# Optimization experiments

Measured on AMD Instinct MI355X. Metric: run time of the kernel, lower is better.

## Reference

```python
import jax, jax.numpy as jnp
import numpy as np

EPS = 1e-5

def setup_inputs() -> dict:
    key = jax.random.key(0)
    k1, k2, k3 = jax.random.split(key, 3)
    B, D, H = 8192, 1536, 16384
    x = jax.random.normal(k1, (B, D), dtype=jnp.float32)
    # torch Linear default init ~ U(-1/sqrt(fan_in), 1/sqrt(fan_in)); scaled normal is fine for a reference
    W_enc = jax.random.normal(k2, (H, D), dtype=jnp.float32) * (1.0 / np.sqrt(D))
    W_dec = jax.random.normal(k3, (D, H), dtype=jnp.float32) * (1.0 / np.sqrt(H))
    pre_bias = jnp.zeros((D,), dtype=jnp.float32)
    latent_bias = jnp.zeros((H,), dtype=jnp.float32)
    return {"x": x, "W_enc": W_enc, "W_dec": W_dec,
            "pre_bias": pre_bias, "latent_bias": latent_bias, "k": 64}


def reference(x, W_enc, W_dec, pre_bias, latent_bias, k):
    # ---- LN preprocess (torch .std uses Bessel correction, ddof=1) ----
    mu = jnp.mean(x, axis=-1, keepdims=True)          # [B,1]
    xc = x - mu
    std = jnp.std(xc, axis=-1, keepdims=True, ddof=1)  # [B,1]
    xn = xc / (std + EPS)

    # ---- encode: Linear(bias=False) on (xn - pre_bias), add latent_bias ----
    h = jnp.einsum('bd,hd->bh', xn - pre_bias, W_enc) + latent_bias  # [B,H]
    h = jax.nn.relu(h)

    # ---- topk sparsity: keep values >= k-th largest per row ----
    topk_vals = jax.lax.top_k(h, k)[0]                # [B,k]
    threshold = topk_vals[:, -1:]                     # [B,1]
    h_sparse = h * (h >= threshold)

    # ---- decode + denormalize ----
    recon = jnp.einsum('bh,dh->bd', h_sparse, W_dec) + pre_bias
    recon = recon * std + mu

    # ---- metrics (as arrays instead of .item()) ----
    sparsity_ratio = jnp.mean(jnp.mean((h_sparse == 0).astype(jnp.float32), axis=1))
    abs_h = jnp.abs(h_sparse)
    mean_activation = jnp.mean(abs_h)
    std_activation = jnp.std(abs_h, ddof=1)
    return recon, h_sparse, sparsity_ratio, mean_activation, std_activation
```

## Files before the change

kernel.cpp:

```cpp
#include <hip/hip_runtime.h>
#include <hip/hip_bf16.h>
#include <math.h>

static constexpr int Bn = 8192;
static constexpr int Hn = 16384;
static constexpr int Dn = 1536;
static constexpr int KTOP = 64;
static constexpr int KE = 1536;
static constexpr int WSTR = 2048;
static constexpr double EPSD = 1e-5;

static constexpr size_t MU_OFF  = 0;
static constexpr size_t STD_OFF = 32768;
static constexpr size_t CNT_OFF = 98304;
static constexpr size_t NNZ_OFF = 131072;
static constexpr size_t SUM_OFF = 131200;
static constexpr size_t MUD_OFF = 262144;
static constexpr size_t RID_OFF = 327680;
static constexpr size_t IDX_OFF = (size_t)1 << 20;
static constexpr size_t VAL_OFF = (size_t)6 << 20;
static constexpr size_t AP_OFF  = (size_t)16 << 20;
static constexpr size_t BP_OFF  = (size_t)48 << 20;
static constexpr size_t WT_OFF  = (size_t)104 << 20;
static constexpr size_t H16_OFF = (size_t)176 << 20;

typedef __attribute__((ext_vector_type(8))) short short8;
typedef __attribute__((ext_vector_type(4))) float f32x4;

static __device__ __forceinline__ unsigned short f2bf(float f) {
    __hip_bfloat16 b = __float2bfloat16(f);
    return *reinterpret_cast<unsigned short*>(&b);
}
static __device__ __forceinline__ float bf2f(unsigned short u) {
    return __uint_as_float(((unsigned)u) << 16);
}
static __device__ __forceinline__ void gload_lds16(const void* g, void* l) {
    __builtin_amdgcn_global_load_lds(
        (const __attribute__((address_space(1))) unsigned int*)g,
        (__attribute__((address_space(3))) unsigned int*)l, 16, 0, 0);
}

__global__ void k_zero(unsigned* nnz, double* sums) {
    if (threadIdx.x == 0) { *nnz = 0u; sums[0] = 0.0; sums[1] = 0.0; }
}

__global__ __launch_bounds__(256) void k_rowstats(const float* __restrict__ x,
                                                  const float* __restrict__ pre_bias,
                                                  double* __restrict__ muD,
                                                  double* __restrict__ rinvD,
                                                  float* __restrict__ muF,
                                                  float* __restrict__ stdF,
                                                  unsigned short* __restrict__ Ap) {
    const int row = blockIdx.x;
    const int tid = threadIdx.x;
    const float* xr = x + (size_t)row * Dn;
    float v[6];
#pragma unroll
    for (int i = 0; i < 6; ++i) v[i] = xr[tid + 256 * i];
    double s = 0.0;
#pragma unroll
    for (int i = 0; i < 6; ++i) s += (double)v[i];
    __shared__ double redD[4];
    __shared__ double smu, srin;
#pragma unroll
    for (int o = 32; o > 0; o >>= 1) s += __shfl_down(s, o);
    if ((tid & 63) == 0) redD[tid >> 6] = s;
    __syncthreads();
    if (tid == 0) smu = (redD[0] + redD[1] + redD[2] + redD[3]) / (double)Dn;
    __syncthreads();
    const double m = smu;
    double q = 0.0;
#pragma unroll
    for (int i = 0; i < 6; ++i) { double d = (double)v[i] - m; q += d * d; }
#pragma unroll
    for (int o = 32; o > 0; o >>= 1) q += __shfl_down(q, o);
    if ((tid & 63) == 0) redD[tid >> 6] = q;
    __syncthreads();
    if (tid == 0) {
        double var = (redD[0] + redD[1] + redD[2] + redD[3]) / (double)(Dn - 1);
        double sd = sqrt(var);
        muD[row] = m;
        srin = 1.0 / (sd + EPSD);
        rinvD[row] = srin;
        muF[row] = (float)m;
        stdF[row] = (float)sd;
    }
    __syncthreads();
    const double ri = srin;
    unsigned short* ar = Ap + (size_t)row * KE;
#pragma unroll
    for (int i = 0; i < 6; ++i) {
        const int d = tid + i * 256;
        double a = ((double)v[i] - m) * ri - (double)pre_bias[d];
        ar[d] = f2bf((float)a);
    }
}

__global__ __launch_bounds__(256) void k_splitW(const float* __restrict__ Wenc,
                                                unsigned short* __restrict__ Bp) {
    const int row = blockIdx.x;
    const int tid = threadIdx.x;
    const float2* wr = (const float2*)(Wenc + (size_t)row * Dn);
    ushort2* br = (ushort2*)(Bp + (size_t)row * KE);
#pragma unroll
    for (int i = 0; i < 3; ++i) {
        float2 w = wr[tid + i * 256];
        ushort2 o; o.x = f2bf(w.x); o.y = f2bf(w.y);
        br[tid + i * 256] = o;
    }
}

__global__ __launch_bounds__(256) void k_transpose(const float* __restrict__ Wdec,
                                                   unsigned short* __restrict__ WdecT) {
    __shared__ float tile[32][33];
    const int h0 = blockIdx.x * 32;
    const int d0 = blockIdx.y * 32;
    const int tx = threadIdx.x & 31;
    const int ty = threadIdx.x >> 5;
#pragma unroll
    for (int r = 0; r < 4; ++r) {
        int d = ty + r * 8;
        tile[d][tx] = Wdec[(size_t)(d0 + d) * Hn + h0 + tx];
    }
    __syncthreads();
#pragma unroll
    for (int r = 0; r < 4; ++r) {
        int h = ty + r * 8;
        WdecT[(size_t)(h0 + h) * WSTR + d0 + tx] = f2bf(tile[tx][h]);
    }
}

__global__ __launch_bounds__(256) void k_gemm(const unsigned short* __restrict__ Ap,
                                              const unsigned short* __restrict__ Bp,
                                              const float* __restrict__ lat_bias,
                                              unsigned short* __restrict__ hout16) {
    __shared__ unsigned short As[128 * 64];
    __shared__ unsigned short Bs[128 * 64];
    const int tid = threadIdx.x;
    const int lane = tid & 63;
    const int w = tid >> 6;
    const int wm = w >> 1, wn = w & 1;

    const int nwg = (Bn / 128) * (Hn / 128);
    int swz = (blockIdx.x % 8) * (nwg / 8) + blockIdx.x / 8;
    int st = swz >> 6;
    int wi = swz & 63;
    int stm = st >> 4, stn = st & 15;
    const int bm = stm * 8 + (wi >> 3);
    const int bn = stn * 8 + (wi & 7);

    const int sr = tid >> 3;
    const int sp = tid & 7;
    const int ssl = sp ^ (sr & 7);
    const size_t arow0 = (size_t)(bm * 128) * KE;
    const size_t brow0 = (size_t)(bn * 128) * KE;

    f32x4 acc[4][4];
#pragma unroll
    for (int i = 0; i < 4; ++i)
#pragma unroll
        for (int j = 0; j < 4; ++j) acc[i][j] = (f32x4){0.f, 0.f, 0.f, 0.f};

    constexpr int NT = KE / 64;
    for (int t = 0; t < NT; ++t) {
        const int k0 = t * 64;
#pragma unroll
        for (int i = 0; i < 4; ++i) {
            gload_lds16(Ap + arow0 + (size_t)(i * 32 + sr) * KE + k0 + ssl * 8,
                        (char*)As + i * 4096 + tid * 16);
            gload_lds16(Bp + brow0 + (size_t)(i * 32 + sr) * KE + k0 + ssl * 8,
                        (char*)Bs + i * 4096 + tid * 16);
        }
        __syncthreads();
#pragma unroll
        for (int kk = 0; kk < 2; ++kk) {
            short8 af[4], bf[4];
#pragma unroll
            for (int f = 0; f < 4; ++f) {
                const int ar = wm * 64 + f * 16 + (lane & 15);
                const int aslot = (kk * 4 + (lane >> 4)) ^ (ar & 7);
                af[f] = *(const short8*)((const char*)As + ar * 128 + aslot * 16);
                const int brr = wn * 64 + f * 16 + (lane & 15);
                const int bslot = (kk * 4 + (lane >> 4)) ^ (brr & 7);
                bf[f] = *(const short8*)((const char*)Bs + brr * 128 + bslot * 16);
            }
#pragma unroll
            for (int fi = 0; fi < 4; ++fi)
#pragma unroll
                for (int fj = 0; fj < 4; ++fj)
                    acc[fi][fj] = __builtin_amdgcn_mfma_f32_16x16x32_bf16(
                        af[fi], bf[fj], acc[fi][fj], 0, 0, 0);
        }
        __syncthreads();
    }

    const int col = lane & 15;
    float biasv[4];
#pragma unroll
    for (int fj = 0; fj < 4; ++fj)
        biasv[fj] = lat_bias[bn * 128 + wn * 64 + fj * 16 + col];
#pragma unroll
    for (int fi = 0; fi < 4; ++fi) {
        const int gm0 = bm * 128 + wm * 64 + fi * 16 + (lane >> 4) * 4;
#pragma unroll
        for (int fj = 0; fj < 4; ++fj) {
            const int gn = bn * 128 + wn * 64 + fj * 16 + col;
#pragma unroll
            for (int r = 0; r < 4; ++r) {
                float vv = acc[fi][fj][r] + biasv[fj];
                hout16[(size_t)(gm0 + r) * Hn + gn] = f2bf(fmaxf(vv, 0.f));
            }
        }
    }
}

__global__ __launch_bounds__(256) void k_topsel(const unsigned short* __restrict__ h16,
                                                const float* __restrict__ x,
                                                const float* __restrict__ Wenc,
                                                const float* __restrict__ pre_bias,
                                                const float* __restrict__ lat_bias,
                                                const double* __restrict__ muD,
                                                const double* __restrict__ rinvD,
                                                unsigned* __restrict__ counts,
                                                int* __restrict__ idx_list,
                                                float* __restrict__ val_list) {
    const int row = blockIdx.x;
    const int tid = threadIdx.x;
    const int lane = tid & 63;
    const int wid = tid >> 6;
    const unsigned short* hr16 = h16 + (size_t)row * Hn;
    const unsigned* hu = (const unsigned*)hr16;
    unsigned u[32];
#pragma unroll
    for (int j = 0; j < 32; ++j) u[j] = hu[j * 256 + tid];

    __shared__ int wsum[4];
    __shared__ unsigned sbc;
    unsigned lo = 0, hi = 0xFFFFu;
    while (lo < hi) {
        const unsigned mid = (lo + hi + 1) >> 1;
        int c = 0;
#pragma unroll
        for (int j = 0; j < 32; ++j) {
            c += ((u[j] & 0xFFFFu) >= mid) ? 1 : 0;
            c += ((u[j] >> 16) >= mid) ? 1 : 0;
        }
#pragma unroll
        for (int o = 32; o > 0; o >>= 1) c += __shfl_down(c, o);
        if ((tid & 63) == 0) wsum[tid >> 6] = c;
        __syncthreads();
        if (tid == 0) sbc = (unsigned)(wsum[0] + wsum[1] + wsum[2] + wsum[3]);
        __syncthreads();
        if (sbc >= (unsigned)KTOP) lo = mid; else hi = mid - 1;
    }
    const float thr = bf2f((unsigned short)lo);
    const float DELTA = 0.02f;
    const float hi_t = thr + DELTA;
    const float lo_t = thr - DELTA;

    constexpr int MAXC = 128;
    __shared__ int s_g, s_c;
    __shared__ int cidx[MAXC];
    __shared__ double cvalD[MAXC];
    __shared__ float cref[MAXC];
    __shared__ unsigned char csel[MAXC];
    __shared__ unsigned long long kmask[256];
    __shared__ unsigned ccnt[256];
    __shared__ unsigned cinc[256];
    if (tid == 0) { s_g = 0; s_c = 0; }
    __syncthreads();
    int g_loc = 0;
#pragma unroll
    for (int j = 0; j < 32; ++j) {
        float v0 = bf2f((unsigned short)(u[j] & 0xFFFFu));
        float v1 = bf2f((unsigned short)(u[j] >> 16));
        const int i0 = 2 * (j * 256 + tid);
        if (v0 > hi_t) g_loc++;
        else if (v0 >= lo_t) {
            int p = atomicAdd(&s_c, 1);
            if (p < MAXC) cidx[p] = i0;
        }
        if (v1 > hi_t) g_loc++;
        else if (v1 >= lo_t) {
            int p = atomicAdd(&s_c, 1);
            if (p < MAXC) cidx[p] = i0 + 1;
        }
    }
    if (g_loc) atomicAdd(&s_g, g_loc);
    __syncthreads();
    const int ec = (s_c < MAXC) ? s_c : MAXC;

    {
        const double rmu = muD[row];
        const double rin = rinvD[row];
        const float* xr = x + (size_t)row * Dn;
        for (int e = wid; e < ec; e += 4) {
            const int feat = cidx[e];
            const float* wr = Wenc + (size_t)feat * Dn;
            double acc = 0.0;
            for (int d = lane; d < Dn; d += 64) {
                double xn = ((double)xr[d] - rmu) * rin - (double)pre_bias[d];
                acc = fma(xn, (double)wr[d], acc);
            }
#pragma unroll
            for (int o = 32; o > 0; o >>= 1) acc += __shfl_down(acc, o);
            if (lane == 0) {
                double hv = acc + (double)lat_bias[feat];
                cvalD[e] = hv;
                float hf = (float)hv;
                cref[e] = hf > 0.f ? hf : 0.f;
            }
        }
    }
    __syncthreads();
    if (tid == 0) {
        const int need = KTOP - s_g;
        for (int e = 0; e < ec; ++e) csel[e] = 0;
        for (int it = 0; it < need && it < ec; ++it) {
            int best = -1; double bv = -1e300; int bidx = 1 << 30;
            for (int e = 0; e < ec; ++e) {
                if (csel[e]) continue;
                if (cvalD[e] > bv || (cvalD[e] == bv && cidx[e] < bidx)) {
                    bv = cvalD[e]; best = e; bidx = cidx[e];
                }
            }
            if (best >= 0) csel[best] = 1;
        }
    }
    __syncthreads();

    for (int i = 0; i < 64; ++i) {
        const int c = wid * 64 + i;
        const int f = c * 64 + lane;
        float val = bf2f(hr16[f]);
        bool keep;
        if (val > hi_t) keep = true;
        else if (val >= lo_t) {
            keep = false;
            for (int e = 0; e < ec; ++e)
                if (cidx[e] == f) { keep = (csel[e] != 0); break; }
        } else keep = false;
        unsigned long long bm = __ballot(keep);
        if (lane == 0) { kmask[c] = bm; ccnt[c] = (unsigned)__popcll(bm); }
    }
    __syncthreads();
    cinc[tid] = ccnt[tid];
    __syncthreads();
#pragma unroll
    for (int o = 1; o < 256; o <<= 1) {
        unsigned t = cinc[tid] + ((tid >= o) ? cinc[tid - o] : 0u);
        __syncthreads();
        cinc[tid] = t;
        __syncthreads();
    }
    if (tid == 0) {
        unsigned tot = cinc[255];
        counts[row] = tot < 128u ? tot : 128u;
    }
    __syncthreads();
    for (int i = 0; i < 64; ++i) {
        const int c = wid * 64 + i;
        unsigned long long bm = kmask[c];
        if (!bm) continue;
        bool keep = (bm >> lane) & 1ull;
        if (keep) {
            unsigned pos = (cinc[c] - ccnt[c]) +
                           (unsigned)__popcll(bm & ((1ull << lane) - 1ull));
            if (pos < 128u) {
                const int f = c * 64 + lane;
                float sv = bf2f(hr16[f]);
                if (sv >= lo_t && sv <= hi_t) {
                    for (int e = 0; e < ec; ++e)
                        if (cidx[e] == f) { sv = cref[e]; break; }
                }
                idx_list[(size_t)row * 128 + pos] = f;
                val_list[(size_t)row * 128 + pos] = sv;
            }
        }
    }
}

__global__ __launch_bounds__(256) void k_hwrite(const unsigned* __restrict__ counts,
                                                const int* __restrict__ idx_list,
                                                const float* __restrict__ val_list,
                                                float* __restrict__ outh,
                                                unsigned* __restrict__ nnz_acc,
                                                double* __restrict__ sums) {
    const int row = blockIdx.x;
    const int tid = threadIdx.x;
    const unsigned cnt = counts[row];
    float* orow = outh + (size_t)row * Hn;
    float4* orow16 = (float4*)orow;
    const float4 z = {0.f, 0.f, 0.f, 0.f};
#pragma unroll
    for (int i = 0; i < 16; ++i) orow16[tid + i * 256] = z;
    __syncthreads();
    float val = 0.f;
    if (tid < (int)cnt) {
        int idx = idx_list[(size_t)row * 128 + tid];
        val = val_list[(size_t)row * 128 + tid];
        orow[idx] = val;
    }
    float s1 = val, s2 = val * val;
    __shared__ float r1[4], r2[4];
#pragma unroll
    for (int o = 32; o > 0; o >>= 1) {
        s1 += __shfl_down(s1, o);
        s2 += __shfl_down(s2, o);
    }
    if ((tid & 63) == 0) { r1[tid >> 6] = s1; r2[tid >> 6] = s2; }
    __syncthreads();
    if (tid == 0) {
        atomicAdd(sums + 0, (double)(r1[0] + r1[1] + r1[2] + r1[3]));
        atomicAdd(sums + 1, (double)(r2[0] + r2[1] + r2[2] + r2[3]));
        atomicAdd(nnz_acc, cnt);
    }
}

__global__ __launch_bounds__(256) void k_decoder(const unsigned short* __restrict__ WdecT,
                                                 const float* __restrict__ pre_bias,
                                                 const float* __restrict__ muF,
                                                 const float* __restrict__ stdF,
                                                 const unsigned* __restrict__ counts,
                                                 const int* __restrict__ idx_list,
                                                 const float* __restrict__ val_list,
                                                 float* __restrict__ outr) {
    const int row = blockIdx.x;
    const int tid = threadIdx.x;
    const unsigned cnt = counts[row];
    __shared__ int sidx[128];
    __shared__ float sval[128];
    if (tid < (int)cnt) {
        sidx[tid] = idx_list[(size_t)row * 128 + tid];
        sval[tid] = val_list[(size_t)row * 128 + tid];
    }
    __syncthreads();
    if (tid >= 192) return;

    float a[8] = {0.f, 0.f, 0.f, 0.f, 0.f, 0.f, 0.f, 0.f};
    float b[8] = {0.f, 0.f, 0.f, 0.f, 0.f, 0.f, 0.f, 0.f};
    const size_t toff = (size_t)tid * 8;
    unsigned j = 0;
    for (; j + 2 <= cnt; j += 2) {
        short8 w0 = *(const short8*)(WdecT + (size_t)sidx[j] * WSTR + toff);
        short8 w1 = *(const short8*)(WdecT + (size_t)sidx[j + 1] * WSTR + toff);
        const float v0 = sval[j], v1 = sval[j + 1];
#pragma unroll
        for (int i = 0; i < 8; ++i) {
            a[i] = fmaf(v0, bf2f((unsigned short)w0[i]), a[i]);
            b[i] = fmaf(v1, bf2f((unsigned short)w1[i]), b[i]);
        }
    }
    if (j < cnt) {
        short8 w0 = *(const short8*)(WdecT + (size_t)sidx[j] * WSTR + toff);
        const float v0 = sval[j];
#pragma unroll
        for (int i = 0; i < 8; ++i)
            a[i] = fmaf(v0, bf2f((unsigned short)w0[i]), a[i]);
    }
    const float m_ = muF[row], s_ = stdF[row];
    const int d0 = tid * 8;
    float o[8];
#pragma unroll
    for (int i = 0; i < 8; ++i)
        o[i] = ((a[i] + b[i]) + pre_bias[d0 + i]) * s_ + m_;
    float* orow = outr + (size_t)row * Dn + d0;
    *(float4*)(orow)     = *(float4*)&o[0];
    *(float4*)(orow + 4) = *(float4*)&o[4];
}

__global__ void k_final(const unsigned* __restrict__ nnz,
                        const double* __restrict__ sums,
                        float* __restrict__ out3) {
    if (threadIdx.x == 0) {
        const double N = (double)Bn * (double)Hn;
        const double nz = (double)(*nnz);
        const double sparsity = (N - nz) / N;
        const double mean = sums[0] / N;
        double var = (sums[1] - N * mean * mean) / (N - 1.0);
        if (var < 0.0) var = 0.0;
        out3[0] = (float)sparsity;
        out3[1] = (float)mean;
        out3[2] = (float)sqrt(var);
    }
}

extern "C" void kernel_launch(void* const* d_in, const int* in_sizes, int n_in,
                              void* d_out, int out_size, void* d_ws, size_t ws_size,
                              hipStream_t stream) {
    const float* x        = (const float*)d_in[0];
    const float* Wenc     = (const float*)d_in[1];
    const float* Wdec     = (const float*)d_in[2];
    const float* pre_bias = (const float*)d_in[3];
    const float* lat_bias = (const float*)d_in[4];

    char* ws = (char*)d_ws;
    float*          muF    = (float*)(ws + MU_OFF);
    float*          stdF   = (float*)(ws + STD_OFF);
    unsigned*       counts = (unsigned*)(ws + CNT_OFF);
    unsigned*       nnz    = (unsigned*)(ws + NNZ_OFF);
    double*         sums   = (double*)(ws + SUM_OFF);
    double*         muD    = (double*)(ws + MUD_OFF);
    double*         rinvD  = (double*)(ws + RID_OFF);
    int*            idxl   = (int*)(ws + IDX_OFF);
    float*          vall   = (float*)(ws + VAL_OFF);
    unsigned short* Ap     = (unsigned short*)(ws + AP_OFF);
    unsigned short* Bp     = (unsigned short*)(ws + BP_OFF);
    unsigned short* WdecT  = (unsigned short*)(ws + WT_OFF);
    unsigned short* h16    = (unsigned short*)(ws + H16_OFF);

    float* out       = (float*)d_out;
    float* out_recon = out;
    float* out_h     = out + (size_t)Bn * Dn;
    float* out_sc    = out + (size_t)Bn * Dn + (size_t)Bn * Hn;

    hipLaunchKernelGGL(k_zero, dim3(1), dim3(64), 0, stream, nnz, sums);
    hipLaunchKernelGGL(k_rowstats, dim3(Bn), dim3(256), 0, stream,
                       x, pre_bias, muD, rinvD, muF, stdF, Ap);
    hipLaunchKernelGGL(k_splitW, dim3(Hn), dim3(256), 0, stream, Wenc, Bp);
    hipLaunchKernelGGL(k_transpose, dim3(Hn / 32, Dn / 32), dim3(256), 0, stream, Wdec, WdecT);
    hipLaunchKernelGGL(k_gemm, dim3((Bn / 128) * (Hn / 128)), dim3(256), 0, stream,
                       Ap, Bp, lat_bias, h16);
    hipLaunchKernelGGL(k_topsel, dim3(Bn), dim3(256), 0, stream,
                       h16, x, Wenc, pre_bias, lat_bias, muD, rinvD,
                       counts, idxl, vall);
    hipLaunchKernelGGL(k_hwrite, dim3(Bn), dim3(256), 0, stream,
                       counts, idxl, vall, out_h, nnz, sums);
    hipLaunchKernelGGL(k_decoder, dim3(Bn), dim3(256), 0, stream,
                       WdecT, pre_bias, muF, stdF, counts, idxl, vall, out_recon);
    hipLaunchKernelGGL(k_final, dim3(1), dim3(64), 0, stream, nnz, sums, out_sc);
}
```

Measured before the change: 1.602 ms.

## Enlarge encoder GEMM tile to 256x256 with double-buffered LDS prefetch

The encoder GEMM moves from 128x128 tiles with 4 waves to 256x256 tiles with 8 waves, so each wave computes a 128x64 sub-tile. LDS is double-buffered and the next K-tile is prefetched two steps ahead, with explicit vmcnt waits and barriers so loads overlap the MFMA work. This targets global-load latency and raises data reuse per LDS byte. In exchange it needs 128KB of LDS per block and more accumulator registers, which can lower occupancy; the launch bound of two blocks per CU may not be reachable.

After: 1.456 ms. -9.1%, faster.

```diff
diff --git a/kernel.cpp b/kernel.cpp
--- a/kernel.cpp
+++ b/kernel.cpp
@@ -130,84 +130,113 @@
     }
 }
 
-__global__ __launch_bounds__(256) void k_gemm(const unsigned short* __restrict__ Ap,
-                                              const unsigned short* __restrict__ Bp,
-                                              const float* __restrict__ lat_bias,
-                                              unsigned short* __restrict__ hout16) {
-    __shared__ unsigned short As[128 * 64];
-    __shared__ unsigned short Bs[128 * 64];
+__global__ __launch_bounds__(512, 2) void k_gemm(const unsigned short* __restrict__ Ap,
+                                                 const unsigned short* __restrict__ Bp,
+                                                 const float* __restrict__ lat_bias,
+                                                 unsigned short* __restrict__ hout16) {
+    __shared__ unsigned short AsBuf[2][256 * 64];
+    __shared__ unsigned short BsBuf[2][256 * 64];
     const int tid = threadIdx.x;
     const int lane = tid & 63;
     const int w = tid >> 6;
-    const int wm = w >> 1, wn = w & 1;
-
-    const int nwg = (Bn / 128) * (Hn / 128);
+    const int wm = w >> 2;
+    const int wn = w & 3;
+
+    const int nwg = (Bn / 256) * (Hn / 256);
     int swz = (blockIdx.x % 8) * (nwg / 8) + blockIdx.x / 8;
     int st = swz >> 6;
     int wi = swz & 63;
-    int stm = st >> 4, stn = st & 15;
+    int stm = st >> 3, stn = st & 7;
     const int bm = stm * 8 + (wi >> 3);
     const int bn = stn * 8 + (wi & 7);
 
-    const int sr = tid >> 3;
-    const int sp = tid & 7;
-    const int ssl = sp ^ (sr & 7);
-    const size_t arow0 = (size_t)(bm * 128) * KE;
-    const size_t brow0 = (size_t)(bn * 128) * KE;
-
-    f32x4 acc[4][4];
-#pragma unroll
-    for (int i = 0; i < 4; ++i)
+    const size_t arow0 = (size_t)(bm * 256) * KE;
+    const size_t brow0 = (size_t)(bn * 256) * KE;
+
+    #define STAGE_TILE(kt, buf)                                                   \
+        {                                                                         \
+            _Pragma("unroll")                                                     \
+            for (int l = 0; l < 4; ++l) {                                         \
+                const int idx = l * 512 + tid;                                    \
+                const int row = idx >> 3, slot = idx & 7;                         \
+                const int ssl = slot ^ (row & 7);                                 \
+                gload_lds16(Ap + arow0 + (size_t)row * KE + (kt) * 64 + ssl * 8,  \
+                            (char*)AsBuf[buf] + idx * 16);                        \
+                gload_lds16(Bp + brow0 + (size_t)row * KE + (kt) * 64 + ssl * 8,  \
+                            (char*)BsBuf[buf] + idx * 16);                        \
+            }                                                                     \
+        }
+
+    f32x4 acc[8][4];
+#pragma unroll
+    for (int i = 0; i < 8; ++i)
 #pragma unroll
         for (int j = 0; j < 4; ++j) acc[i][j] = (f32x4){0.f, 0.f, 0.f, 0.f};
 
     constexpr int NT = KE / 64;
+    STAGE_TILE(0, 0);
+    STAGE_TILE(1, 1);
+    asm volatile("s_waitcnt vmcnt(8)" ::: "memory");
+    __builtin_amdgcn_s_barrier();
+    asm volatile("" ::: "memory");
+
     for (int t = 0; t < NT; ++t) {
-        const int k0 = t * 64;
-#pragma unroll
-        for (int i = 0; i < 4; ++i) {
-            gload_lds16(Ap + arow0 + (size_t)(i * 32 + sr) * KE + k0 + ssl * 8,
-                        (char*)As + i * 4096 + tid * 16);
-            gload_lds16(Bp + brow0 + (size_t)(i * 32 + sr) * KE + k0 + ssl * 8,
-                        (char*)Bs + i * 4096 + tid * 16);
-        }
-        __syncthreads();
-#pragma unroll
-        for (int kk = 0; kk < 2; ++kk) {
-            short8 af[4], bf[4];
-#pragma unroll
-            for (int f = 0; f < 4; ++f) {
-                const int ar = wm * 64 + f * 16 + (lane & 15);
-                const int aslot = (kk * 4 + (lane >> 4)) ^ (ar & 7);
-                af[f] = *(const short8*)((const char*)As + ar * 128 + aslot * 16);
-                const int brr = wn * 64 + f * 16 + (lane & 15);
-                const int bslot = (kk * 4 + (lane >> 4)) ^ (brr & 7);
-                bf[f] = *(const short8*)((const char*)Bs + brr * 128 + bslot * 16);
+        const int buf = t & 1;
+        const unsigned short* Ab = AsBuf[buf];
+        const unsigned short* Bb = BsBuf[buf];
+        short8 bfr[4][2];
+#pragma unroll
+        for (int fj = 0; fj < 4; ++fj)
+#pragma unroll
+            for (int kk = 0; kk < 2; ++kk) {
+                const int br = wn * 64 + fj * 16 + (lane & 15);
+                const int slot = (kk * 4 + (lane >> 4)) ^ (br & 7);
+                bfr[fj][kk] = *(const short8*)((const char*)Bb + br * 128 + slot * 16);
             }
 #pragma unroll
+        for (int qm = 0; qm < 2; ++qm) {
+            short8 afr[4][2];
+#pragma unroll
             for (int fi = 0; fi < 4; ++fi)
 #pragma unroll
-                for (int fj = 0; fj < 4; ++fj)
-                    acc[fi][fj] = __builtin_amdgcn_mfma_f32_16x16x32_bf16(
-                        af[fi], bf[fj], acc[fi][fj], 0, 0, 0);
-        }
-        __syncthreads();
-    }
+                for (int kk = 0; kk < 2; ++kk) {
+                    const int ar = wm * 128 + qm * 64 + fi * 16 + (lane & 15);
+                    const int slot = (kk * 4 + (lane >> 4)) ^ (ar & 7);
+                    afr[fi][kk] = *(const short8*)((const char*)Ab + ar * 128 + slot * 16);
+                }
+#pragma unroll
+            for (int kk = 0; kk < 2; ++kk)
+#pragma unroll
+                for (int fi = 0; fi < 4; ++fi)
+#pragma unroll
+                    for (int fj = 0; fj < 4; ++fj)
+                        acc[qm * 4 + fi][fj] = __builtin_amdgcn_mfma_f32_16x16x32_bf16(
+                            afr[fi][kk], bfr[fj][kk], acc[qm * 4 + fi][fj], 0, 0, 0);
+        }
+        __builtin_amdgcn_s_barrier();
+        asm volatile("" ::: "memory");
+        if (t + 2 < NT) {
+            STAGE_TILE(t + 2, buf);
+            asm volatile("s_waitcnt vmcnt(8)" ::: "memory");
+        } else {
+            asm volatile("s_waitcnt vmcnt(0)" ::: "memory");
+        }
+        __builtin_amdgcn_s_barrier();
+        asm volatile("" ::: "memory");
+    }
+    #undef STAGE_TILE
 
     const int col = lane & 15;
-    float biasv[4];
-#pragma unroll
-    for (int fj = 0; fj < 4; ++fj)
-        biasv[fj] = lat_bias[bn * 128 + wn * 64 + fj * 16 + col];
-#pragma unroll
-    for (int fi = 0; fi < 4; ++fi) {
-        const int gm0 = bm * 128 + wm * 64 + fi * 16 + (lane >> 4) * 4;
-#pragma unroll
-        for (int fj = 0; fj < 4; ++fj) {
-            const int gn = bn * 128 + wn * 64 + fj * 16 + col;
+#pragma unroll
+    for (int fj = 0; fj < 4; ++fj) {
+        const int gn = bn * 256 + wn * 64 + fj * 16 + col;
+        const float bias = lat_bias[gn];
+#pragma unroll
+        for (int fi8 = 0; fi8 < 8; ++fi8) {
+            const int gm0 = bm * 256 + wm * 128 + fi8 * 16 + (lane >> 4) * 4;
 #pragma unroll
             for (int r = 0; r < 4; ++r) {
-                float vv = acc[fi][fj][r] + biasv[fj];
+                float vv = acc[fi8][fj][r] + bias;
                 hout16[(size_t)(gm0 + r) * Hn + gn] = f2bf(fmaxf(vv, 0.f));
             }
         }
@@ -519,7 +548,7 @@
                        x, pre_bias, muD, rinvD, muF, stdF, Ap);
     hipLaunchKernelGGL(k_splitW, dim3(Hn), dim3(256), 0, stream, Wenc, Bp);
     hipLaunchKernelGGL(k_transpose, dim3(Hn / 32, Dn / 32), dim3(256), 0, stream, Wdec, WdecT);
-    hipLaunchKernelGGL(k_gemm, dim3((Bn / 128) * (Hn / 128)), dim3(256), 0, stream,
+    hipLaunchKernelGGL(k_gemm, dim3((Bn / 256) * (Hn / 256)), dim3(512), 0, stream,
                        Ap, Bp, lat_bias, h16);
     hipLaunchKernelGGL(k_topsel, dim3(Bn), dim3(256), 0, stream,
                        h16, x, Wenc, pre_bias, lat_bias, muD, rinvD,
```
